# Kernel optimization log

Measured on AMD Instinct MI355X. Metric: run time of the kernel, lower is better.

The kernel has to match this reference:

```python
import jax, jax.numpy as jnp
import numpy as np

IN_DIM = 256
BOTTLENECK = 32
QK_DIM = IN_DIM // BOTTLENECK  # 8


def setup_inputs() -> dict:
    key = jax.random.key(0)
    ks = jax.random.split(key, 10)
    B, C, W, H = 4, IN_DIM, 64, 64
    s = 0.05
    return {
        "x": jax.random.normal(ks[0], (B, C, W, H), jnp.float32),
        "k": jax.random.normal(ks[1], (B, C, W, H), jnp.float32),
        "q": jax.random.normal(ks[2], (B, C, W, H), jnp.float32),
        "Wq": jax.random.normal(ks[3], (QK_DIM, C), jnp.float32) * s,
        "bq": jax.random.normal(ks[4], (QK_DIM,), jnp.float32) * s,
        "Wk": jax.random.normal(ks[5], (QK_DIM, C), jnp.float32) * s,
        "bk": jax.random.normal(ks[6], (QK_DIM,), jnp.float32) * s,
        "Wv": jax.random.normal(ks[7], (C, C), jnp.float32) * s,
        "bv": jax.random.normal(ks[8], (C,), jnp.float32) * s,
        "gamma": jnp.array([0.5], jnp.float32),
    }


def reference(x, k, q, Wq, bq, Wk, bk, Wv, bv, gamma):
    B, C, W, H = x.shape
    N = W * H
    # 1x1 convs == per-pixel linear maps over channels; flatten spatial to N
    xf = x.reshape(B, C, N)
    kf = k.reshape(B, C, N)
    qf = q.reshape(B, C, N)
    # proj_query: (B, N, d); proj_key: (B, d, N)
    pq = jnp.einsum('dc,bcn->bnd', Wq, qf) + bq[None, None, :]
    pk = jnp.einsum('dc,bcn->bdn', Wk, kf) + bk[None, :, None]
    energy = jnp.einsum('bnd,bdm->bnm', pq, pk)  # (B, N, N), un-scaled
    attention = jax.nn.softmax(energy, axis=-1)
    pv = jnp.einsum('ec,bcn->ben', Wv, xf) + bv[None, :, None]  # (B, C, N)
    # out = bmm(value, attention^T): out[b,c,n] = sum_m pv[b,c,m] * attn[b,n,m]
    out = jnp.einsum('bcm,bnm->bcn', pv, attention)
    out = out.reshape(B, C, W, H)
    out = gamma[0] * out + x
    return out, attention
```

## Files before the change

### kernel.cpp

```cpp
#include <hip/hip_runtime.h>

#define B_ 4
#define C_ 256
#define N_ 4096
#define D_ 8

typedef float f32x4 __attribute__((ext_vector_type(4)));
typedef __bf16 bf16x8 __attribute__((ext_vector_type(8)));

union U16 {
  bf16x8 v;
  unsigned short u[8];
  uint4 q;
};

__device__ inline unsigned short f2bf(float f) {
  unsigned int u = __float_as_uint(f);
  u = (u + 0x7FFFu + ((u >> 16) & 1u)) >> 16;
  return (unsigned short)u;
}

#define AS1 __attribute__((address_space(1)))
#define AS3 __attribute__((address_space(3)))
__device__ __forceinline__ void g2l16(const void* g, void* l) {
  __builtin_amdgcn_global_load_lds((AS1 const void*)g, (AS3 void*)l, 16, 0, 0);
}

__global__ void __launch_bounds__(256) k_pqk(
    const float* __restrict__ q, const float* __restrict__ k,
    const float* __restrict__ Wq, const float* __restrict__ bq,
    const float* __restrict__ Wk, const float* __restrict__ bk,
    float* __restrict__ pq_g, float* __restrict__ pk_g) {
  int b = blockIdx.y, n0 = blockIdx.x * 64;
  int t = threadIdx.x, nl = t & 63, sub = t >> 6;
  int n = n0 + nl;
  float aq[D_], ak[D_];
#pragma unroll
  for (int d = 0; d < D_; ++d) { aq[d] = 0.f; ak[d] = 0.f; }
  const float* qp = q + ((size_t)(b * C_ + sub * 64)) * N_ + n;
  const float* kp = k + ((size_t)(b * C_ + sub * 64)) * N_ + n;
  for (int cc = 0; cc < 64; ++cc) {
    int c = sub * 64 + cc;
    float qv = qp[(size_t)cc * N_];
    float kv = kp[(size_t)cc * N_];
#pragma unroll
    for (int d = 0; d < D_; ++d) {
      aq[d] = fmaf(Wq[d * C_ + c], qv, aq[d]);
      ak[d] = fmaf(Wk[d * C_ + c], kv, ak[d]);
    }
  }
  __shared__ float red[4][64][16];
#pragma unroll
  for (int d = 0; d < D_; ++d) { red[sub][nl][d] = aq[d]; red[sub][nl][8 + d] = ak[d]; }
  __syncthreads();
  if (t < 64) {
#pragma unroll
    for (int d = 0; d < D_; ++d) {
      float s = red[0][t][d] + red[1][t][d] + red[2][t][d] + red[3][t][d] + bq[d];
      pq_g[((size_t)b * N_ + n0 + t) * D_ + d] = s;
      float s2 = red[0][t][8 + d] + red[1][t][8 + d] + red[2][t][8 + d] + red[3][t][8 + d] + bk[d];
      pk_g[((size_t)b * D_ + d) * N_ + n0 + t] = s2;
    }
  }
}

__global__ void __launch_bounds__(256) k_pv(
    const float* __restrict__ x, const float* __restrict__ Wv,
    const float* __restrict__ bv, unsigned short* __restrict__ pv_g) {
  int b = blockIdx.y, n0 = blockIdx.x * 64;
  int t = threadIdx.x, lane = t & 63, w = t >> 6;
  __shared__ unsigned short xs[64][264];
  {
    int nl = t & 63, sub = t >> 6;
    for (int i = 0; i < 64; ++i) {
      int c = i * 4 + sub;
      float xv = x[((size_t)(b * C_ + c)) * N_ + n0 + nl];
      xs[nl][c] = f2bf(xv);
    }
  }
  __syncthreads();
  int e0 = w * 64;
  f32x4 acc[4][4];
#pragma unroll
  for (int mf = 0; mf < 4; ++mf)
#pragma unroll
    for (int nf = 0; nf < 4; ++nf) acc[mf][nf] = (f32x4)0.f;

  int rsel = lane & 15, koff = (lane >> 4) * 8;
  for (int kc = 0; kc < 8; ++kc) {
    int cbase = kc * 32 + koff;
    U16 afr[4];
#pragma unroll
    for (int mf = 0; mf < 4; ++mf) {
      const float* wp = Wv + (size_t)(e0 + mf * 16 + rsel) * C_ + cbase;
      float4 w0 = *(const float4*)wp;
      float4 w1 = *(const float4*)(wp + 4);
      afr[mf].u[0] = f2bf(w0.x); afr[mf].u[1] = f2bf(w0.y);
      afr[mf].u[2] = f2bf(w0.z); afr[mf].u[3] = f2bf(w0.w);
      afr[mf].u[4] = f2bf(w1.x); afr[mf].u[5] = f2bf(w1.y);
      afr[mf].u[6] = f2bf(w1.z); afr[mf].u[7] = f2bf(w1.w);
    }
    U16 bfr[4];
#pragma unroll
    for (int nf = 0; nf < 4; ++nf)
      bfr[nf].q = *(const uint4*)&xs[nf * 16 + rsel][cbase];
#pragma unroll
    for (int mf = 0; mf < 4; ++mf)
#pragma unroll
      for (int nf = 0; nf < 4; ++nf)
        acc[mf][nf] = __builtin_amdgcn_mfma_f32_16x16x32_bf16(afr[mf].v, bfr[nf].v, acc[mf][nf], 0, 0, 0);
  }
  int rowsub = (lane >> 4) * 4;
#pragma unroll
  for (int mf = 0; mf < 4; ++mf) {
#pragma unroll
    for (int nf = 0; nf < 4; ++nf) {
      int n = n0 + nf * 16 + rsel;
#pragma unroll
      for (int j = 0; j < 4; ++j) {
        int e = e0 + mf * 16 + rowsub + j;
        float v = acc[mf][nf][j] + bv[e];
        pv_g[((size_t)(b * C_ + e)) * N_ + n] = f2bf(v);
      }
    }
  }
}

__global__ void __launch_bounds__(256) k_rowsum(
    const float* __restrict__ pq_g, const float* __restrict__ pk_g,
    float* __restrict__ rinv_g) {
  int b = blockIdx.y, n0 = blockIdx.x * 32;
  int t = threadIdx.x, lane = t & 63, w = t >> 6;
  int r0 = n0 + w * 8;
  float pqr[8][D_];
#pragma unroll
  for (int r = 0; r < 8; ++r) {
    const float4* pp = (const float4*)(pq_g + ((size_t)b * N_ + r0 + r) * D_);
    float4 a = pp[0], c4 = pp[1];
    pqr[r][0] = a.x; pqr[r][1] = a.y; pqr[r][2] = a.z; pqr[r][3] = a.w;
    pqr[r][4] = c4.x; pqr[r][5] = c4.y; pqr[r][6] = c4.z; pqr[r][7] = c4.w;
  }
  float s[8];
#pragma unroll
  for (int r = 0; r < 8; ++r) s[r] = 0.f;
  const float* pkb = pk_g + (size_t)b * D_ * N_;
  for (int tt = 0; tt < 64; ++tt) {
    int m = tt * 64 + lane;
    float pkr[D_];
#pragma unroll
    for (int d = 0; d < D_; ++d) pkr[d] = pkb[(size_t)d * N_ + m];
#pragma unroll
    for (int r = 0; r < 8; ++r) {
      float e = pqr[r][0] * pkr[0];
#pragma unroll
      for (int d = 1; d < D_; ++d) e = fmaf(pqr[r][d], pkr[d], e);
      s[r] += __expf(e);
    }
  }
#pragma unroll
  for (int r = 0; r < 8; ++r) {
    float v = s[r];
    for (int off = 32; off; off >>= 1) v += __shfl_xor(v, off);
    s[r] = v;
  }
  if (lane == 0) {
#pragma unroll
    for (int r = 0; r < 8; ++r) rinv_g[(size_t)b * N_ + r0 + r] = 1.0f / s[r];
  }
}

__global__ void __launch_bounds__(256, 2) k_fused(
    const float* __restrict__ pq_g, const float* __restrict__ pk_g,
    const float* __restrict__ rinv_g, const unsigned short* __restrict__ pv_g,
    const float* __restrict__ x, const float* __restrict__ gamma,
    float* __restrict__ out_g, float* __restrict__ attn_g) {
  int bx = blockIdx.x;
  int b = bx & 3, grp = bx >> 2;
  int n0 = grp * 32;
  int t = threadIdx.x, lane = t & 63, w = t >> 6;
  int rsel = lane & 15, g = lane >> 4, koff = g * 8;
  int c0 = w * 64;
  int r0 = n0 + w * 8;

  __shared__ unsigned short pvs[2][256][64];
  __shared__ unsigned short asl[2][32][72];

  float pqr[8][D_], rinv[8];
#pragma unroll
  for (int rr = 0; rr < 8; ++rr) {
    const float4* pp = (const float4*)(pq_g + ((size_t)b * N_ + r0 + rr) * D_);
    float4 a = pp[0], c4 = pp[1];
    pqr[rr][0] = a.x; pqr[rr][1] = a.y; pqr[rr][2] = a.z; pqr[rr][3] = a.w;
    pqr[rr][4] = c4.x; pqr[rr][5] = c4.y; pqr[rr][6] = c4.z; pqr[rr][7] = c4.w;
    rinv[rr] = rinv_g[(size_t)b * N_ + r0 + rr];
  }

  const float* pkb = pk_g + (size_t)b * D_ * N_;
  const unsigned short* pvb = pv_g + (size_t)b * C_ * N_;
  float* attb = attn_g + ((size_t)b * N_ + r0) * N_;

  f32x4 acc[2][4];
#pragma unroll
  for (int mf = 0; mf < 2; ++mf)
#pragma unroll
    for (int cf = 0; cf < 4; ++cf) acc[mf][cf] = (f32x4)0.f;

#define STAGEPV(dstbuf, M0)                                                   \
  {                                                                           \
    _Pragma("unroll")                                                         \
    for (int i = 0; i < 8; ++i) {                                             \
      int c = c0 + i * 8 + (lane >> 3);                                       \
      int seg = lane & 7;                                                     \
      g2l16(pvb + (size_t)c * N_ + (M0) + ((seg ^ (c & 7)) << 3),             \
            &pvs[dstbuf][c0 + i * 8][0]);                                     \
    }                                                                         \
  }

  STAGEPV(0, 0)
  float pkr[D_];
#pragma unroll
  for (int d = 0; d < D_; ++d) pkr[d] = pkb[(size_t)d * N_ + lane];

  int cur = 0;
  for (int tt = 0; tt < 64; ++tt) {
    int m0 = tt * 64;
    bool more = (tt + 1 < 64);
    if (more) STAGEPV(cur ^ 1, m0 + 64)
    float pkn[D_];
    if (more) {
#pragma unroll
      for (int d = 0; d < D_; ++d) pkn[d] = pkb[(size_t)d * N_ + m0 + 64 + lane];
    }
#pragma unroll
    for (int rr = 0; rr < 8; ++rr) {
      float e = pqr[rr][0] * pkr[0];
#pragma unroll
      for (int d = 1; d < D_; ++d) e = fmaf(pqr[rr][d], pkr[d], e);
      float a = __expf(e) * rinv[rr];
      __builtin_nontemporal_store(a, attb + (size_t)rr * N_ + m0 + lane);
      asl[cur][w * 8 + rr][lane] = f2bf(a);
    }
    asm volatile("s_waitcnt lgkmcnt(0)" ::: "memory");
    __builtin_amdgcn_s_barrier();
    {
      U16 afr[2][2], bfr[2][4];
#pragma unroll
      for (int kf = 0; kf < 2; ++kf) {
#pragma unroll
        for (int mf = 0; mf < 2; ++mf)
          afr[kf][mf].q = *(const uint4*)&asl[cur][mf * 16 + rsel][kf * 32 + koff];
#pragma unroll
        for (int cf = 0; cf < 4; ++cf) {
          int c = c0 + cf * 16 + rsel;
          int sg = kf * 4 + g;
          bfr[kf][cf].q = *(const uint4*)&pvs[cur][c][(sg ^ (c & 7)) * 8];
        }
      }
#pragma unroll
      for (int kf = 0; kf < 2; ++kf)
#pragma unroll
        for (int mf = 0; mf < 2; ++mf)
#pragma unroll
          for (int cf = 0; cf < 4; ++cf)
            acc[mf][cf] = __builtin_amdgcn_mfma_f32_16x16x32_bf16(
                afr[kf][mf].v, bfr[kf][cf].v, acc[mf][cf], 0, 0, 0);
    }
#pragma unroll
    for (int d = 0; d < D_; ++d) pkr[d] = pkn[d];
    cur ^= 1;
  }
#undef STAGEPV
  float gm = gamma[0];
  int rowsub = g * 4;
#pragma unroll
  for (int mf = 0; mf < 2; ++mf) {
#pragma unroll
    for (int cf = 0; cf < 4; ++cf) {
      int c = c0 + cf * 16 + rsel;
      int nrow = n0 + mf * 16 + rowsub;
      const float4 xv = *(const float4*)(x + ((size_t)(b * C_ + c)) * N_ + nrow);
      float4 o;
      o.x = gm * acc[mf][cf][0] + xv.x;
      o.y = gm * acc[mf][cf][1] + xv.y;
      o.z = gm * acc[mf][cf][2] + xv.z;
      o.w = gm * acc[mf][cf][3] + xv.w;
      *(float4*)(out_g + ((size_t)(b * C_ + c)) * N_ + nrow) = o;
    }
  }
}

extern "C" void kernel_launch(void* const* d_in, const int* in_sizes, int n_in,
                              void* d_out, int out_size, void* d_ws, size_t ws_size,
                              hipStream_t stream) {
  const float* x  = (const float*)d_in[0];
  const float* k  = (const float*)d_in[1];
  const float* q  = (const float*)d_in[2];
  const float* Wq = (const float*)d_in[3];
  const float* bq = (const float*)d_in[4];
  const float* Wk = (const float*)d_in[5];
  const float* bk = (const float*)d_in[6];
  const float* Wv = (const float*)d_in[7];
  const float* bv = (const float*)d_in[8];
  const float* gamma = (const float*)d_in[9];

  float* out_g  = (float*)d_out;
  float* attn_g = out_g + (size_t)B_ * C_ * N_;

  char* ws = (char*)d_ws;
  float* pq_g = (float*)ws;
  float* pk_g = (float*)(ws + (1u << 19));
  float* rinv_g = (float*)(ws + (1u << 20));
  unsigned short* pv_g = (unsigned short*)(ws + (1u << 20) + (1u << 17));

  k_pqk<<<dim3(64, B_), 256, 0, stream>>>(q, k, Wq, bq, Wk, bk, pq_g, pk_g);
  k_pv<<<dim3(64, B_), 256, 0, stream>>>(x, Wv, bv, pv_g);
  k_rowsum<<<dim3(128, B_), 256, 0, stream>>>(pq_g, pk_g, rinv_g);
  k_fused<<<dim3(512), 256, 0, stream>>>(pq_g, pk_g, rinv_g, pv_g, x, gamma, out_g, attn_g);
}
```

Measured before the change: 161.0 us.

## Split attention-store work into separate blocks interleaved with MFMA blocks in one kernel

```diff
diff --git a/kernel.cpp b/kernel.cpp
--- a/kernel.cpp
+++ b/kernel.cpp
@@ -169,41 +169,43 @@
   }
 }
 
-__global__ void __launch_bounds__(256, 2) k_fused(
+__global__ void __launch_bounds__(256, 2) k_mega(
     const float* __restrict__ pq_g, const float* __restrict__ pk_g,
     const float* __restrict__ rinv_g, const unsigned short* __restrict__ pv_g,
     const float* __restrict__ x, const float* __restrict__ gamma,
     float* __restrict__ out_g, float* __restrict__ attn_g) {
-  int bx = blockIdx.x;
-  int b = bx & 3, grp = bx >> 2;
-  int n0 = grp * 32;
-  int t = threadIdx.x, lane = t & 63, w = t >> 6;
-  int rsel = lane & 15, g = lane >> 4, koff = g * 8;
-  int c0 = w * 64;
-  int r0 = n0 + w * 8;
-
   __shared__ unsigned short pvs[2][256][64];
   __shared__ unsigned short asl[2][32][72];
 
-  float pqr[8][D_], rinv[8];
-#pragma unroll
-  for (int rr = 0; rr < 8; ++rr) {
-    const float4* pp = (const float4*)(pq_g + ((size_t)b * N_ + r0 + rr) * D_);
-    float4 a = pp[0], c4 = pp[1];
-    pqr[rr][0] = a.x; pqr[rr][1] = a.y; pqr[rr][2] = a.z; pqr[rr][3] = a.w;
-    pqr[rr][4] = c4.x; pqr[rr][5] = c4.y; pqr[rr][6] = c4.z; pqr[rr][7] = c4.w;
-    rinv[rr] = rinv_g[(size_t)b * N_ + r0 + rr];
-  }
-
-  const float* pkb = pk_g + (size_t)b * D_ * N_;
-  const unsigned short* pvb = pv_g + (size_t)b * C_ * N_;
-  float* attb = attn_g + ((size_t)b * N_ + r0) * N_;
-
-  f32x4 acc[2][4];
-#pragma unroll
-  for (int mf = 0; mf < 2; ++mf)
-#pragma unroll
-    for (int cf = 0; cf < 4; ++cf) acc[mf][cf] = (f32x4)0.f;
+  int bx = blockIdx.x;
+  int r5 = bx % 5, q5 = bx / 5;
+  int t = threadIdx.x, lane = t & 63, w = t >> 6;
+
+  if (r5 == 4) {
+    int b = q5 & 3, grp = q5 >> 2;
+    int n0 = grp * 32;
+    int rsel = lane & 15, g = lane >> 4, koff = g * 8;
+    int c0 = w * 64;
+    int r0 = n0 + w * 8;
+
+    float pqr[8][D_], rinv[8];
+#pragma unroll
+    for (int rr = 0; rr < 8; ++rr) {
+      const float4* pp = (const float4*)(pq_g + ((size_t)b * N_ + r0 + rr) * D_);
+      float4 a = pp[0], c4 = pp[1];
+      pqr[rr][0] = a.x; pqr[rr][1] = a.y; pqr[rr][2] = a.z; pqr[rr][3] = a.w;
+      pqr[rr][4] = c4.x; pqr[rr][5] = c4.y; pqr[rr][6] = c4.z; pqr[rr][7] = c4.w;
+      rinv[rr] = rinv_g[(size_t)b * N_ + r0 + rr];
+    }
+
+    const float* pkb = pk_g + (size_t)b * D_ * N_;
+    const unsigned short* pvb = pv_g + (size_t)b * C_ * N_;
+
+    f32x4 acc[2][4];
+#pragma unroll
+    for (int mf = 0; mf < 2; ++mf)
+#pragma unroll
+      for (int cf = 0; cf < 4; ++cf) acc[mf][cf] = (f32x4)0.f;
 
 #define STAGEPV(dstbuf, M0)                                                   \
   {                                                                           \
@@ -216,75 +218,110 @@
     }                                                                         \
   }
 
-  STAGEPV(0, 0)
-  float pkr[D_];
-#pragma unroll
-  for (int d = 0; d < D_; ++d) pkr[d] = pkb[(size_t)d * N_ + lane];
-
-  int cur = 0;
-  for (int tt = 0; tt < 64; ++tt) {
-    int m0 = tt * 64;
-    bool more = (tt + 1 < 64);
-    if (more) STAGEPV(cur ^ 1, m0 + 64)
-    float pkn[D_];
-    if (more) {
-#pragma unroll
-      for (int d = 0; d < D_; ++d) pkn[d] = pkb[(size_t)d * N_ + m0 + 64 + lane];
-    }
+    STAGEPV(0, 0)
+    float pkr[D_];
+#pragma unroll
+    for (int d = 0; d < D_; ++d) pkr[d] = pkb[(size_t)d * N_ + lane];
+
+    int cur = 0;
+    for (int tt = 0; tt < 64; ++tt) {
+      int m0 = tt * 64;
+      bool more = (tt + 1 < 64);
+      if (more) STAGEPV(cur ^ 1, m0 + 64)
+      float pkn[D_];
+      if (more) {
+#pragma unroll
+        for (int d = 0; d < D_; ++d) pkn[d] = pkb[(size_t)d * N_ + m0 + 64 + lane];
+      }
+#pragma unroll
+      for (int rr = 0; rr < 8; ++rr) {
+        float e = pqr[rr][0] * pkr[0];
+#pragma unroll
+        for (int d = 1; d < D_; ++d) e = fmaf(pqr[rr][d], pkr[d], e);
+        float a = __expf(e) * rinv[rr];
+        asl[cur][w * 8 + rr][lane] = f2bf(a);
+      }
+      asm volatile("s_waitcnt lgkmcnt(0)" ::: "memory");
+      __builtin_amdgcn_s_barrier();
+      {
+        U16 afr[2][2], bfr[2][4];
+#pragma unroll
+        for (int kf = 0; kf < 2; ++kf) {
+#pragma unroll
+          for (int mf = 0; mf < 2; ++mf)
+            afr[kf][mf].q = *(const uint4*)&asl[cur][mf * 16 + rsel][kf * 32 + koff];
+#pragma unroll
+          for (int cf = 0; cf < 4; ++cf) {
+            int c = c0 + cf * 16 + rsel;
+            int sg = kf * 4 + g;
+            bfr[kf][cf].q = *(const uint4*)&pvs[cur][c][(sg ^ (c & 7)) * 8];
+          }
+        }
+#pragma unroll
+        for (int kf = 0; kf < 2; ++kf)
+#pragma unroll
+          for (int mf = 0; mf < 2; ++mf)
+#pragma unroll
+            for (int cf = 0; cf < 4; ++cf)
+              acc[mf][cf] = __builtin_amdgcn_mfma_f32_16x16x32_bf16(
+                  afr[kf][mf].v, bfr[kf][cf].v, acc[mf][cf], 0, 0, 0);
+      }
+#pragma unroll
+      for (int d = 0; d < D_; ++d) pkr[d] = pkn[d];
+      cur ^= 1;
+    }
+#undef STAGEPV
+    float gm = gamma[0];
+    int rowsub = g * 4;
+#pragma unroll
+    for (int mf = 0; mf < 2; ++mf) {
+#pragma unroll
+      for (int cf = 0; cf < 4; ++cf) {
+        int c = c0 + cf * 16 + rsel;
+        int nrow = n0 + mf * 16 + rowsub;
+        const float4 xv = *(const float4*)(x + ((size_t)(b * C_ + c)) * N_ + nrow);
+        float4 o;
+        o.x = gm * acc[mf][cf][0] + xv.x;
+        o.y = gm * acc[mf][cf][1] + xv.y;
+        o.z = gm * acc[mf][cf][2] + xv.z;
+        o.w = gm * acc[mf][cf][3] + xv.w;
+        *(float4*)(out_g + ((size_t)(b * C_ + c)) * N_ + nrow) = o;
+      }
+    }
+  } else {
+    int aid = q5 * 4 + r5;
+    int b = aid & 3;
+    int rg = aid >> 2;
+    int r0 = rg * 8;
+    int mq = w * 1024;
+
+    float pqr[8][D_];
 #pragma unroll
     for (int rr = 0; rr < 8; ++rr) {
-      float e = pqr[rr][0] * pkr[0];
-#pragma unroll
-      for (int d = 1; d < D_; ++d) e = fmaf(pqr[rr][d], pkr[d], e);
-      float a = __expf(e) * rinv[rr];
-      __builtin_nontemporal_store(a, attb + (size_t)rr * N_ + m0 + lane);
-      asl[cur][w * 8 + rr][lane] = f2bf(a);
-    }
-    asm volatile("s_waitcnt lgkmcnt(0)" ::: "memory");
-    __builtin_amdgcn_s_barrier();
-    {
-      U16 afr[2][2], bfr[2][4];
-#pragma unroll
-      for (int kf = 0; kf < 2; ++kf) {
-#pragma unroll
-        for (int mf = 0; mf < 2; ++mf)
-          afr[kf][mf].q = *(const uint4*)&asl[cur][mf * 16 + rsel][kf * 32 + koff];
-#pragma unroll
-        for (int cf = 0; cf < 4; ++cf) {
-          int c = c0 + cf * 16 + rsel;
-          int sg = kf * 4 + g;
-          bfr[kf][cf].q = *(const uint4*)&pvs[cur][c][(sg ^ (c & 7)) * 8];
-        }
-      }
-#pragma unroll
-      for (int kf = 0; kf < 2; ++kf)
-#pragma unroll
-        for (int mf = 0; mf < 2; ++mf)
-#pragma unroll
-          for (int cf = 0; cf < 4; ++cf)
-            acc[mf][cf] = __builtin_amdgcn_mfma_f32_16x16x32_bf16(
-                afr[kf][mf].v, bfr[kf][cf].v, acc[mf][cf], 0, 0, 0);
-    }
-#pragma unroll
-    for (int d = 0; d < D_; ++d) pkr[d] = pkn[d];
-    cur ^= 1;
-  }
-#undef STAGEPV
-  float gm = gamma[0];
-  int rowsub = g * 4;
-#pragma unroll
-  for (int mf = 0; mf < 2; ++mf) {
-#pragma unroll
-    for (int cf = 0; cf < 4; ++cf) {
-      int c = c0 + cf * 16 + rsel;
-      int nrow = n0 + mf * 16 + rowsub;
-      const float4 xv = *(const float4*)(x + ((size_t)(b * C_ + c)) * N_ + nrow);
-      float4 o;
-      o.x = gm * acc[mf][cf][0] + xv.x;
-      o.y = gm * acc[mf][cf][1] + xv.y;
-      o.z = gm * acc[mf][cf][2] + xv.z;
-      o.w = gm * acc[mf][cf][3] + xv.w;
-      *(float4*)(out_g + ((size_t)(b * C_ + c)) * N_ + nrow) = o;
+      const float4* pp = (const float4*)(pq_g + ((size_t)b * N_ + r0 + rr) * D_);
+      float4 a = pp[0], c4 = pp[1];
+      pqr[rr][0] = a.x; pqr[rr][1] = a.y; pqr[rr][2] = a.z; pqr[rr][3] = a.w;
+      pqr[rr][4] = c4.x; pqr[rr][5] = c4.y; pqr[rr][6] = c4.z; pqr[rr][7] = c4.w;
+    }
+    const float* pkb = pk_g + (size_t)b * D_ * N_;
+    float rinv[8];
+#pragma unroll
+    for (int rr = 0; rr < 8; ++rr) rinv[rr] = rinv_g[(size_t)b * N_ + r0 + rr];
+
+    float* attb = attn_g + ((size_t)b * N_ + r0) * N_;
+    for (int tt = 0; tt < 16; ++tt) {
+      int m = mq + tt * 64 + lane;
+      float pkr[D_];
+#pragma unroll
+      for (int d = 0; d < D_; ++d) pkr[d] = pkb[(size_t)d * N_ + m];
+#pragma unroll
+      for (int rr = 0; rr < 8; ++rr) {
+        float e = pqr[rr][0] * pkr[0];
+#pragma unroll
+        for (int d = 1; d < D_; ++d) e = fmaf(pqr[rr][d], pkr[d], e);
+        float a = __expf(e) * rinv[rr];
+        __builtin_nontemporal_store(a, attb + (size_t)rr * N_ + m);
+      }
     }
   }
 }
@@ -315,5 +352,5 @@
   k_pqk<<<dim3(64, B_), 256, 0, stream>>>(q, k, Wq, bq, Wk, bk, pq_g, pk_g);
   k_pv<<<dim3(64, B_), 256, 0, stream>>>(x, Wv, bv, pv_g);
   k_rowsum<<<dim3(128, B_), 256, 0, stream>>>(pq_g, pk_g, rinv_g);
-  k_fused<<<dim3(512), 256, 0, stream>>>(pq_g, pk_g, rinv_g, pv_g, x, gamma, out_g, attn_g);
-}
+  k_mega<<<dim3(2560), 256, 0, stream>>>(pq_g, pk_g, rinv_g, pv_g, x, gamma, out_g, attn_g);
+}
```

New measurement: 229.0 us. 42.3% more time.
